# Kernel tuning notes

Measured on AMD Instinct MI355X. Metric: run time of the kernel, lower is better.

Reference implementation:

```python
import jax, jax.numpy as jnp
from jax import lax
import numpy as np

T, B, C, H = 2048, 512, 8, 20  # seq_len, batch, input channels, hidden size


def _lstm_layer(x_seq, W_ih, W_hh, b_ih, b_hh):
    """One unidirectional LSTM layer, PyTorch gate order (i, f, g, o).
    x_seq: [T, B, in], W_ih: [4H, in], W_hh: [4H, H]. Returns h sequence [T, B, H]."""
    Hh = W_hh.shape[1]
    # Precompute input contribution for all timesteps (batched GEMM, off the scan critical path)
    gx = jnp.einsum('tbc,gc->tbg', x_seq, W_ih) + b_ih + b_hh  # [T, B, 4H]

    def step(carry, g_t):
        h, c = carry
        g = g_t + h @ W_hh.T  # [B, 4H]
        i, f, gg, o = jnp.split(g, 4, axis=-1)
        i = jax.nn.sigmoid(i)
        f = jax.nn.sigmoid(f)
        gg = jnp.tanh(gg)
        o = jax.nn.sigmoid(o)
        c = f * c + i * gg
        h = o * jnp.tanh(c)
        return (h, c), h

    b = x_seq.shape[1]
    h0 = jnp.zeros((b, Hh), x_seq.dtype)
    c0 = jnp.zeros((b, Hh), x_seq.dtype)
    _, ys = lax.scan(step, (h0, c0), gx)
    return ys


def setup_inputs() -> dict:
    key = jax.random.key(0)
    ks = jax.random.split(key, 9)
    s = 1.0 / np.sqrt(H)  # PyTorch LSTM init scale
    return {
        'x': jax.random.normal(ks[0], (T, B, C), jnp.float32),
        'W_ih0': jax.random.uniform(ks[1], (4 * H, C), jnp.float32, -s, s),
        'W_hh0': jax.random.uniform(ks[2], (4 * H, H), jnp.float32, -s, s),
        'b_ih0': jax.random.uniform(ks[3], (4 * H,), jnp.float32, -s, s),
        'b_hh0': jax.random.uniform(ks[4], (4 * H,), jnp.float32, -s, s),
        'W_ih1': jax.random.uniform(ks[5], (4 * H, H), jnp.float32, -s, s),
        'W_hh1': jax.random.uniform(ks[6], (4 * H, H), jnp.float32, -s, s),
        'b_ih1': jax.random.uniform(ks[7], (4 * H,), jnp.float32, -s, s),
        'b_hh1': jax.random.uniform(ks[8], (4 * H,), jnp.float32, -s, s),
    }


def reference(x, W_ih0, W_hh0, b_ih0, b_hh0, W_ih1, W_hh1, b_ih1, b_hh1):
    # 2-layer LSTM with zero initial states; forward returns the full output sequence
    # (the fc head in the original module is unused in forward()).
    h1 = _lstm_layer(x, W_ih0, W_hh0, b_ih0, b_hh0)   # [T, B, H]
    out = _lstm_layer(h1, W_ih1, W_hh1, b_ih1, b_hh1)  # [T, B, H]
    return out
```

## Files before the change

kernel.cpp:

```cpp
#include <hip/hip_runtime.h>

namespace {

typedef float v2f __attribute__((ext_vector_type(2)));

constexpr int T_SEQ = 2048;
constexpr int B_SZ  = 512;
constexpr int C_IN  = 8;
constexpr int H_SZ  = 20;
constexpr int P_LEN = 16;
constexpr int N_PH  = T_SEQ / P_LEN;
constexpr int RING  = 2 * P_LEN;
constexpr float LOG2E = 1.44269504088896340736f;

__device__ __forceinline__ float rlane(float v, int lane) {
  return __int_as_float(__builtin_amdgcn_readlane(__float_as_int(v), lane));
}

template<int S>
__device__ __forceinline__ float quad_bcast(float v) {
  return __int_as_float(__builtin_amdgcn_update_dpp(
      __float_as_int(v), __float_as_int(v), S * 0x55, 0xF, 0xF, true));
}

__device__ __forceinline__ v2f fma2(v2f a, v2f b, v2f c) {
  return __builtin_elementwise_fma(a, b, c);
}
__device__ __forceinline__ v2f splat2(float s) { v2f r; r.x = s; r.y = s; return r; }
__device__ __forceinline__ v2f zero2() { v2f r; r.x = 0.f; r.y = 0.f; return r; }

__device__ __forceinline__ v2f act2(v2f a, float cm, float am, float ad) {
  float ex = __builtin_amdgcn_exp2f(a.x * cm);
  float ey = __builtin_amdgcn_exp2f(a.y * cm);
  float sx = __builtin_amdgcn_rcpf(1.0f + ex);
  float sy = __builtin_amdgcn_rcpf(1.0f + ey);
  v2f r; r.x = __fmaf_rn(sx, am, ad); r.y = __fmaf_rn(sy, am, ad);
  return r;
}

__device__ __forceinline__ float fast_tanh(float a) {
  float e = __builtin_amdgcn_exp2f(a * (-2.0f * LOG2E));
  float s = __builtin_amdgcn_rcpf(1.0f + e);
  return __fmaf_rn(s, 2.0f, -1.0f);
}

#define H_BCAST(ha, hb, k) (((k) < 16) ? rlane((ha), 4 * (k)) : rlane((hb), 4 * ((k) - 16)))

__global__ __attribute__((amdgpu_flat_work_group_size(128, 128),
                          amdgpu_waves_per_eu(1, 1)))
void lstm2_pk(const float* __restrict__ x,
              const float* __restrict__ Wih0, const float* __restrict__ Whh0,
              const float* __restrict__ bih0, const float* __restrict__ bhh0,
              const float* __restrict__ Wih1, const float* __restrict__ Whh1,
              const float* __restrict__ bih1, const float* __restrict__ bhh1,
              float* __restrict__ out)
{
  __shared__ __align__(16) float hbuf[RING][H_SZ];
  __shared__ __align__(16) float xbuf[2][P_LEN * C_IN];

  const int tid = threadIdx.x;
  const int wv  = tid >> 6;
  const int l   = tid & 63;
  const int b   = blockIdx.x;
  const int k1  = l >> 2;
  const int g   = l & 3;
  const int k2  = 16 + (k1 & 3);
  const int j1  = g * H_SZ + k1;
  const int j2  = g * H_SZ + k2;

  const bool  isg = (g == 2);
  const float cm  = isg ? (-2.0f * LOG2E) : (-LOG2E);
  const float am  = isg ?  2.0f : 1.0f;
  const float ad  = isg ? -1.0f : 0.0f;

  if (wv == 0) {
    v2f wx1[C_IN / 2], wx2[C_IN / 2];
    v2f wh[H_SZ];
#pragma unroll
    for (int t = 0; t < C_IN / 2; ++t) {
      wx1[t].x = Wih0[j1 * C_IN + 2 * t]; wx1[t].y = Wih0[j1 * C_IN + 2 * t + 1];
      wx2[t].x = Wih0[j2 * C_IN + 2 * t]; wx2[t].y = Wih0[j2 * C_IN + 2 * t + 1];
    }
#pragma unroll
    for (int k = 0; k < H_SZ; ++k) {
      wh[k].x = Whh0[j1 * H_SZ + k]; wh[k].y = Whh0[j2 * H_SZ + k];
    }
    v2f bias2; bias2.x = bih0[j1] + bhh0[j1]; bias2.y = bih0[j2] + bhh0[j2];

    float ha = 0.f, ca = 0.f, hb = 0.f, cb = 0.f;

    const float* xl = x + (size_t)(l >> 3) * (B_SZ * C_IN) + b * C_IN + (l & 7);
    const size_t halfph = (size_t)8 * B_SZ * C_IN;
    const size_t phstr  = (size_t)P_LEN * B_SZ * C_IN;

    {
      float v0 = xl[0], v1 = xl[halfph];
      xbuf[0][l] = v0; xbuf[0][64 + l] = v1;
    }
    float n0 = xl[phstr], n1 = xl[phstr + halfph];

    for (int p = 0; p <= N_PH; ++p) {
      if (p < N_PH) {
        const int buf = p & 1;
        float4 xc0 = ((const float4*)&xbuf[buf][0])[0];
        float4 xc1 = ((const float4*)&xbuf[buf][0])[1];
        for (int j = 0; j < P_LEN; ++j) {
          const int n = p * P_LEN + j;
          v2f xp[4];
          xp[0].x = xc0.x; xp[0].y = xc0.y; xp[1].x = xc0.z; xp[1].y = xc0.w;
          xp[2].x = xc1.x; xp[2].y = xc1.y; xp[3].x = xc1.z; xp[3].y = xc1.w;
          if (j + 1 < P_LEN) {
            xc0 = ((const float4*)&xbuf[buf][(j + 1) * C_IN])[0];
            xc1 = ((const float4*)&xbuf[buf][(j + 1) * C_IN])[1];
          }

          v2f A0 = bias2, A1 = zero2();
#pragma unroll
          for (int k = 0; k < H_SZ; k += 2) {
            float h0 = H_BCAST(ha, hb, k);
            float h1 = H_BCAST(ha, hb, k + 1);
            A0 = fma2(wh[k],     splat2(h0), A0);
            A1 = fma2(wh[k + 1], splat2(h1), A1);
          }
          v2f X1 = zero2(), X2 = zero2();
#pragma unroll
          for (int t = 0; t < C_IN / 2; ++t) {
            X1 = fma2(wx1[t], xp[t], X1);
            X2 = fma2(wx2[t], xp[t], X2);
          }
          v2f A = A0 + A1;
          A.x += X1.x + X1.y;
          A.y += X2.x + X2.y;

          v2f act = act2(A, cm, am, ad);
          float iv = quad_bcast<0>(act.x), fv = quad_bcast<1>(act.x);
          float gv = quad_bcast<2>(act.x), ov = quad_bcast<3>(act.x);
          ca = __fmaf_rn(fv, ca, iv * gv);
          ha = ov * fast_tanh(ca);
          iv = quad_bcast<0>(act.y); fv = quad_bcast<1>(act.y);
          gv = quad_bcast<2>(act.y); ov = quad_bcast<3>(act.y);
          cb = __fmaf_rn(fv, cb, iv * gv);
          hb = ov * fast_tanh(cb);

          const int slot = n & (RING - 1);
          if (g == 0) {
            hbuf[slot][k1] = ha;
            if (k1 < 4) hbuf[slot][16 + k1] = hb;
          }
        }
        if (p + 1 < N_PH) { xbuf[(p + 1) & 1][l] = n0; xbuf[(p + 1) & 1][64 + l] = n1; }
        if (p + 2 < N_PH) {
          n0 = xl[(size_t)(p + 2) * phstr];
          n1 = xl[(size_t)(p + 2) * phstr + halfph];
        }
      }
      __syncthreads();
    }
  } else {
    v2f wy1[H_SZ / 2], wy2[H_SZ / 2];
    v2f wq[H_SZ];
#pragma unroll
    for (int t = 0; t < H_SZ / 2; ++t) {
      wy1[t].x = Wih1[j1 * H_SZ + 2 * t]; wy1[t].y = Wih1[j1 * H_SZ + 2 * t + 1];
      wy2[t].x = Wih1[j2 * H_SZ + 2 * t]; wy2[t].y = Wih1[j2 * H_SZ + 2 * t + 1];
    }
#pragma unroll
    for (int k = 0; k < H_SZ; ++k) {
      wq[k].x = Whh1[j1 * H_SZ + k]; wq[k].y = Whh1[j2 * H_SZ + k];
    }
    v2f bias2; bias2.x = bih1[j1] + bhh1[j1]; bias2.y = bih1[j2] + bhh1[j2];

    float ha = 0.f, ca = 0.f, hb = 0.f, cb = 0.f;
    float* op = out + b * H_SZ;

    auto stepW1 = [&](int n, const float4 (&yq)[5]) {
      v2f yp[H_SZ / 2];
      yp[0].x = yq[0].x; yp[0].y = yq[0].y; yp[1].x = yq[0].z; yp[1].y = yq[0].w;
      yp[2].x = yq[1].x; yp[2].y = yq[1].y; yp[3].x = yq[1].z; yp[3].y = yq[1].w;
      yp[4].x = yq[2].x; yp[4].y = yq[2].y; yp[5].x = yq[2].z; yp[5].y = yq[2].w;
      yp[6].x = yq[3].x; yp[6].y = yq[3].y; yp[7].x = yq[3].z; yp[7].y = yq[3].w;
      yp[8].x = yq[4].x; yp[8].y = yq[4].y; yp[9].x = yq[4].z; yp[9].y = yq[4].w;

      v2f Y1a = zero2(), Y1b = zero2(), Y2a = zero2(), Y2b = zero2();
#pragma unroll
      for (int t = 0; t < H_SZ / 2; t += 2) {
        Y1a = fma2(wy1[t],     yp[t],     Y1a);
        Y2a = fma2(wy2[t],     yp[t],     Y2a);
        Y1b = fma2(wy1[t + 1], yp[t + 1], Y1b);
        Y2b = fma2(wy2[t + 1], yp[t + 1], Y2b);
      }
      v2f Q0 = bias2, Q1 = zero2();
#pragma unroll
      for (int k = 0; k < H_SZ; k += 2) {
        float q0 = H_BCAST(ha, hb, k);
        float q1 = H_BCAST(ha, hb, k + 1);
        Q0 = fma2(wq[k],     splat2(q0), Q0);
        Q1 = fma2(wq[k + 1], splat2(q1), Q1);
      }
      v2f A = Q0 + Q1;
      v2f Y1 = Y1a + Y1b, Y2 = Y2a + Y2b;
      A.x += Y1.x + Y1.y;
      A.y += Y2.x + Y2.y;

      v2f act = act2(A, cm, am, ad);
      float iv = quad_bcast<0>(act.x), fv = quad_bcast<1>(act.x);
      float gv = quad_bcast<2>(act.x), ov = quad_bcast<3>(act.x);
      ca = __fmaf_rn(fv, ca, iv * gv);
      ha = ov * fast_tanh(ca);
      iv = quad_bcast<0>(act.y); fv = quad_bcast<1>(act.y);
      gv = quad_bcast<2>(act.y); ov = quad_bcast<3>(act.y);
      cb = __fmaf_rn(fv, cb, iv * gv);
      hb = ov * fast_tanh(cb);

      if (g == 0) {
        op[k1] = ha;
        if (k1 < 4) op[16 + k1] = hb;
      }
      op += B_SZ * H_SZ;
    };

    for (int p = 0; p <= N_PH; ++p) {
      if (p >= 1) {
        const int base = (p - 1) * P_LEN;
        float4 yA[5], yB[5];
        {
          const float4* s = (const float4*)hbuf[base & (RING - 1)];
          yA[0] = s[0]; yA[1] = s[1]; yA[2] = s[2]; yA[3] = s[3]; yA[4] = s[4];
        }
        {
          const float4* s = (const float4*)hbuf[(base + 1) & (RING - 1)];
          yB[0] = s[0]; yB[1] = s[1]; yB[2] = s[2]; yB[3] = s[3]; yB[4] = s[4];
        }
        for (int jj = 0; jj < P_LEN; jj += 2) {
          stepW1(base + jj, yA);
          if (jj + 2 < P_LEN) {
            const float4* s = (const float4*)hbuf[(base + jj + 2) & (RING - 1)];
            yA[0] = s[0]; yA[1] = s[1]; yA[2] = s[2]; yA[3] = s[3]; yA[4] = s[4];
          }
          stepW1(base + jj + 1, yB);
          if (jj + 3 < P_LEN) {
            const float4* s = (const float4*)hbuf[(base + jj + 3) & (RING - 1)];
            yB[0] = s[0]; yB[1] = s[1]; yB[2] = s[2]; yB[3] = s[3]; yB[4] = s[4];
          }
        }
      }
      __syncthreads();
    }
  }
}

}

extern "C" void kernel_launch(void* const* d_in, const int* in_sizes, int n_in,
                              void* d_out, int out_size, void* d_ws, size_t ws_size,
                              hipStream_t stream) {
  const float* x    = (const float*)d_in[0];
  const float* Wih0 = (const float*)d_in[1];
  const float* Whh0 = (const float*)d_in[2];
  const float* bih0 = (const float*)d_in[3];
  const float* bhh0 = (const float*)d_in[4];
  const float* Wih1 = (const float*)d_in[5];
  const float* Whh1 = (const float*)d_in[6];
  const float* bih1 = (const float*)d_in[7];
  const float* bhh1 = (const float*)d_in[8];
  float* out = (float*)d_out;

  hipLaunchKernelGGL(lstm2_pk, dim3(B_SZ), dim3(128), 0, stream,
                     x, Wih0, Whh0, bih0, bhh0, Wih1, Whh1, bih1, bhh1, out);
}
```

Before: 706.8 us.

## Broadcast recurrent hidden state through LDS instead of readlane, lengthen phases

Replaces the per-step readlane broadcasts of the hidden state (20 scalar readlanes per step) with LDS writes and vectorized v2f LDS reads of the previous h. Layer 0 reads it from the ring buffer and layer 1 from a new double-buffered h1buf. Phase length doubles to 32 to halve block barriers. Within one wave the LDS round trip relies on in-order LDS behaviour, and it adds store-to-load latency to the serial recurrence.

New measurement: 761.5 us. +7.7%, slower.

```diff
diff --git a/kernel.cpp b/kernel.cpp
--- a/kernel.cpp
+++ b/kernel.cpp
@@ -8,14 +8,10 @@
 constexpr int B_SZ  = 512;
 constexpr int C_IN  = 8;
 constexpr int H_SZ  = 20;
-constexpr int P_LEN = 16;
+constexpr int P_LEN = 32;
 constexpr int N_PH  = T_SEQ / P_LEN;
 constexpr int RING  = 2 * P_LEN;
 constexpr float LOG2E = 1.44269504088896340736f;
-
-__device__ __forceinline__ float rlane(float v, int lane) {
-  return __int_as_float(__builtin_amdgcn_readlane(__float_as_int(v), lane));
-}
 
 template<int S>
 __device__ __forceinline__ float quad_bcast(float v) {
@@ -26,7 +22,6 @@
 __device__ __forceinline__ v2f fma2(v2f a, v2f b, v2f c) {
   return __builtin_elementwise_fma(a, b, c);
 }
-__device__ __forceinline__ v2f splat2(float s) { v2f r; r.x = s; r.y = s; return r; }
 __device__ __forceinline__ v2f zero2() { v2f r; r.x = 0.f; r.y = 0.f; return r; }
 
 __device__ __forceinline__ v2f act2(v2f a, float cm, float am, float ad) {
@@ -44,18 +39,17 @@
   return __fmaf_rn(s, 2.0f, -1.0f);
 }
 
-#define H_BCAST(ha, hb, k) (((k) < 16) ? rlane((ha), 4 * (k)) : rlane((hb), 4 * ((k) - 16)))
-
 __global__ __attribute__((amdgpu_flat_work_group_size(128, 128),
                           amdgpu_waves_per_eu(1, 1)))
-void lstm2_pk(const float* __restrict__ x,
-              const float* __restrict__ Wih0, const float* __restrict__ Whh0,
-              const float* __restrict__ bih0, const float* __restrict__ bhh0,
-              const float* __restrict__ Wih1, const float* __restrict__ Whh1,
-              const float* __restrict__ bih1, const float* __restrict__ bhh1,
-              float* __restrict__ out)
+void lstm2_lds(const float* __restrict__ x,
+               const float* __restrict__ Wih0, const float* __restrict__ Whh0,
+               const float* __restrict__ bih0, const float* __restrict__ bhh0,
+               const float* __restrict__ Wih1, const float* __restrict__ Whh1,
+               const float* __restrict__ bih1, const float* __restrict__ bhh1,
+               float* __restrict__ out)
 {
   __shared__ __align__(16) float hbuf[RING][H_SZ];
+  __shared__ __align__(16) float h1buf[2][H_SZ];
   __shared__ __align__(16) float xbuf[2][P_LEN * C_IN];
 
   const int tid = threadIdx.x;
@@ -75,72 +69,70 @@
 
   if (wv == 0) {
     v2f wx1[C_IN / 2], wx2[C_IN / 2];
-    v2f wh[H_SZ];
+    v2f wh1[H_SZ / 2], wh2[H_SZ / 2];
 #pragma unroll
     for (int t = 0; t < C_IN / 2; ++t) {
       wx1[t].x = Wih0[j1 * C_IN + 2 * t]; wx1[t].y = Wih0[j1 * C_IN + 2 * t + 1];
       wx2[t].x = Wih0[j2 * C_IN + 2 * t]; wx2[t].y = Wih0[j2 * C_IN + 2 * t + 1];
     }
 #pragma unroll
-    for (int k = 0; k < H_SZ; ++k) {
-      wh[k].x = Whh0[j1 * H_SZ + k]; wh[k].y = Whh0[j2 * H_SZ + k];
-    }
-    v2f bias2; bias2.x = bih0[j1] + bhh0[j1]; bias2.y = bih0[j2] + bhh0[j2];
-
-    float ha = 0.f, ca = 0.f, hb = 0.f, cb = 0.f;
-
-    const float* xl = x + (size_t)(l >> 3) * (B_SZ * C_IN) + b * C_IN + (l & 7);
-    const size_t halfph = (size_t)8 * B_SZ * C_IN;
-    const size_t phstr  = (size_t)P_LEN * B_SZ * C_IN;
-
+    for (int t = 0; t < H_SZ / 2; ++t) {
+      wh1[t].x = Whh0[j1 * H_SZ + 2 * t]; wh1[t].y = Whh0[j1 * H_SZ + 2 * t + 1];
+      wh2[t].x = Whh0[j2 * H_SZ + 2 * t]; wh2[t].y = Whh0[j2 * H_SZ + 2 * t + 1];
+    }
+    const float bs1 = bih0[j1] + bhh0[j1];
+    const float bs2 = bih0[j2] + bhh0[j2];
+
+    float ca = 0.f, cb = 0.f;
+
+    if (l < H_SZ) hbuf[RING - 1][l] = 0.f;
+
+    const float* xl = x + (size_t)(l >> 3) * (B_SZ * C_IN)
+                        + (size_t)b * C_IN + (l & 7);
+    const size_t ustr  = (size_t)8 * B_SZ * C_IN;
+    const size_t phstr = (size_t)P_LEN * B_SZ * C_IN;
     {
-      float v0 = xl[0], v1 = xl[halfph];
-      xbuf[0][l] = v0; xbuf[0][64 + l] = v1;
-    }
-    float n0 = xl[phstr], n1 = xl[phstr + halfph];
+      float a0 = xl[0], a1 = xl[ustr], a2 = xl[2 * ustr], a3 = xl[3 * ustr];
+      xbuf[0][l] = a0; xbuf[0][64 + l] = a1;
+      xbuf[0][128 + l] = a2; xbuf[0][192 + l] = a3;
+    }
+    float xr0 = xl[phstr], xr1 = xl[phstr + ustr],
+          xr2 = xl[phstr + 2 * ustr], xr3 = xl[phstr + 3 * ustr];
 
     for (int p = 0; p <= N_PH; ++p) {
       if (p < N_PH) {
         const int buf = p & 1;
-        float4 xc0 = ((const float4*)&xbuf[buf][0])[0];
-        float4 xc1 = ((const float4*)&xbuf[buf][0])[1];
         for (int j = 0; j < P_LEN; ++j) {
           const int n = p * P_LEN + j;
-          v2f xp[4];
-          xp[0].x = xc0.x; xp[0].y = xc0.y; xp[1].x = xc0.z; xp[1].y = xc0.w;
-          xp[2].x = xc1.x; xp[2].y = xc1.y; xp[3].x = xc1.z; xp[3].y = xc1.w;
-          if (j + 1 < P_LEN) {
-            xc0 = ((const float4*)&xbuf[buf][(j + 1) * C_IN])[0];
-            xc1 = ((const float4*)&xbuf[buf][(j + 1) * C_IN])[1];
-          }
-
-          v2f A0 = bias2, A1 = zero2();
-#pragma unroll
-          for (int k = 0; k < H_SZ; k += 2) {
-            float h0 = H_BCAST(ha, hb, k);
-            float h1 = H_BCAST(ha, hb, k + 1);
-            A0 = fma2(wh[k],     splat2(h0), A0);
-            A1 = fma2(wh[k + 1], splat2(h1), A1);
-          }
-          v2f X1 = zero2(), X2 = zero2();
-#pragma unroll
-          for (int t = 0; t < C_IN / 2; ++t) {
-            X1 = fma2(wx1[t], xp[t], X1);
-            X2 = fma2(wx2[t], xp[t], X2);
-          }
-          v2f A = A0 + A1;
-          A.x += X1.x + X1.y;
-          A.y += X2.x + X2.y;
-
-          v2f act = act2(A, cm, am, ad);
+          const v2f* xp = (const v2f*)&xbuf[buf][j * C_IN];
+          const v2f* hp = (const v2f*)hbuf[(n + RING - 1) & (RING - 1)];
+
+          v2f A0, A1, A2, A3;
+          A0.x = bs1; A0.y = 0.f; A1 = zero2();
+          A2.x = bs2; A2.y = 0.f; A3 = zero2();
+          A0 = fma2(wx1[0], xp[0], A0);  A2 = fma2(wx2[0], xp[0], A2);
+          A1 = fma2(wx1[1], xp[1], A1);  A3 = fma2(wx2[1], xp[1], A3);
+          A0 = fma2(wx1[2], xp[2], A0);  A2 = fma2(wx2[2], xp[2], A2);
+          A1 = fma2(wx1[3], xp[3], A1);  A3 = fma2(wx2[3], xp[3], A3);
+#pragma unroll
+          for (int t = 0; t < H_SZ / 2; t += 2) {
+            A0 = fma2(wh1[t],     hp[t],     A0);
+            A2 = fma2(wh2[t],     hp[t],     A2);
+            A1 = fma2(wh1[t + 1], hp[t + 1], A1);
+            A3 = fma2(wh2[t + 1], hp[t + 1], A3);
+          }
+          v2f S1 = A0 + A1, S2 = A2 + A3;
+          v2f G; G.x = S1.x + S1.y; G.y = S2.x + S2.y;
+
+          v2f act = act2(G, cm, am, ad);
           float iv = quad_bcast<0>(act.x), fv = quad_bcast<1>(act.x);
           float gv = quad_bcast<2>(act.x), ov = quad_bcast<3>(act.x);
           ca = __fmaf_rn(fv, ca, iv * gv);
-          ha = ov * fast_tanh(ca);
+          float ha = ov * fast_tanh(ca);
           iv = quad_bcast<0>(act.y); fv = quad_bcast<1>(act.y);
           gv = quad_bcast<2>(act.y); ov = quad_bcast<3>(act.y);
           cb = __fmaf_rn(fv, cb, iv * gv);
-          hb = ov * fast_tanh(cb);
+          float hb = ov * fast_tanh(cb);
 
           const int slot = n & (RING - 1);
           if (g == 0) {
@@ -148,100 +140,80 @@
             if (k1 < 4) hbuf[slot][16 + k1] = hb;
           }
         }
-        if (p + 1 < N_PH) { xbuf[(p + 1) & 1][l] = n0; xbuf[(p + 1) & 1][64 + l] = n1; }
+        if (p + 1 < N_PH) {
+          const int nb = (p + 1) & 1;
+          xbuf[nb][l] = xr0; xbuf[nb][64 + l] = xr1;
+          xbuf[nb][128 + l] = xr2; xbuf[nb][192 + l] = xr3;
+        }
         if (p + 2 < N_PH) {
-          n0 = xl[(size_t)(p + 2) * phstr];
-          n1 = xl[(size_t)(p + 2) * phstr + halfph];
+          const size_t o = (size_t)(p + 2) * phstr;
+          xr0 = xl[o]; xr1 = xl[o + ustr];
+          xr2 = xl[o + 2 * ustr]; xr3 = xl[o + 3 * ustr];
         }
       }
       __syncthreads();
     }
   } else {
     v2f wy1[H_SZ / 2], wy2[H_SZ / 2];
-    v2f wq[H_SZ];
+    v2f wq1[H_SZ / 2], wq2[H_SZ / 2];
 #pragma unroll
     for (int t = 0; t < H_SZ / 2; ++t) {
       wy1[t].x = Wih1[j1 * H_SZ + 2 * t]; wy1[t].y = Wih1[j1 * H_SZ + 2 * t + 1];
       wy2[t].x = Wih1[j2 * H_SZ + 2 * t]; wy2[t].y = Wih1[j2 * H_SZ + 2 * t + 1];
-    }
-#pragma unroll
-    for (int k = 0; k < H_SZ; ++k) {
-      wq[k].x = Whh1[j1 * H_SZ + k]; wq[k].y = Whh1[j2 * H_SZ + k];
-    }
-    v2f bias2; bias2.x = bih1[j1] + bhh1[j1]; bias2.y = bih1[j2] + bhh1[j2];
-
-    float ha = 0.f, ca = 0.f, hb = 0.f, cb = 0.f;
-    float* op = out + b * H_SZ;
-
-    auto stepW1 = [&](int n, const float4 (&yq)[5]) {
-      v2f yp[H_SZ / 2];
-      yp[0].x = yq[0].x; yp[0].y = yq[0].y; yp[1].x = yq[0].z; yp[1].y = yq[0].w;
-      yp[2].x = yq[1].x; yp[2].y = yq[1].y; yp[3].x = yq[1].z; yp[3].y = yq[1].w;
-      yp[4].x = yq[2].x; yp[4].y = yq[2].y; yp[5].x = yq[2].z; yp[5].y = yq[2].w;
-      yp[6].x = yq[3].x; yp[6].y = yq[3].y; yp[7].x = yq[3].z; yp[7].y = yq[3].w;
-      yp[8].x = yq[4].x; yp[8].y = yq[4].y; yp[9].x = yq[4].z; yp[9].y = yq[4].w;
-
-      v2f Y1a = zero2(), Y1b = zero2(), Y2a = zero2(), Y2b = zero2();
-#pragma unroll
-      for (int t = 0; t < H_SZ / 2; t += 2) {
-        Y1a = fma2(wy1[t],     yp[t],     Y1a);
-        Y2a = fma2(wy2[t],     yp[t],     Y2a);
-        Y1b = fma2(wy1[t + 1], yp[t + 1], Y1b);
-        Y2b = fma2(wy2[t + 1], yp[t + 1], Y2b);
-      }
-      v2f Q0 = bias2, Q1 = zero2();
-#pragma unroll
-      for (int k = 0; k < H_SZ; k += 2) {
-        float q0 = H_BCAST(ha, hb, k);
-        float q1 = H_BCAST(ha, hb, k + 1);
-        Q0 = fma2(wq[k],     splat2(q0), Q0);
-        Q1 = fma2(wq[k + 1], splat2(q1), Q1);
-      }
-      v2f A = Q0 + Q1;
-      v2f Y1 = Y1a + Y1b, Y2 = Y2a + Y2b;
-      A.x += Y1.x + Y1.y;
-      A.y += Y2.x + Y2.y;
-
-      v2f act = act2(A, cm, am, ad);
-      float iv = quad_bcast<0>(act.x), fv = quad_bcast<1>(act.x);
-      float gv = quad_bcast<2>(act.x), ov = quad_bcast<3>(act.x);
-      ca = __fmaf_rn(fv, ca, iv * gv);
-      ha = ov * fast_tanh(ca);
-      iv = quad_bcast<0>(act.y); fv = quad_bcast<1>(act.y);
-      gv = quad_bcast<2>(act.y); ov = quad_bcast<3>(act.y);
-      cb = __fmaf_rn(fv, cb, iv * gv);
-      hb = ov * fast_tanh(cb);
-
-      if (g == 0) {
-        op[k1] = ha;
-        if (k1 < 4) op[16 + k1] = hb;
-      }
-      op += B_SZ * H_SZ;
-    };
+      wq1[t].x = Whh1[j1 * H_SZ + 2 * t]; wq1[t].y = Whh1[j1 * H_SZ + 2 * t + 1];
+      wq2[t].x = Whh1[j2 * H_SZ + 2 * t]; wq2[t].y = Whh1[j2 * H_SZ + 2 * t + 1];
+    }
+    const float bs1 = bih1[j1] + bhh1[j1];
+    const float bs2 = bih1[j2] + bhh1[j2];
+
+    float ca = 0.f, cb = 0.f;
+    float* op = out + (size_t)b * H_SZ;
+
+    if (l < H_SZ) h1buf[1][l] = 0.f;
 
     for (int p = 0; p <= N_PH; ++p) {
       if (p >= 1) {
         const int base = (p - 1) * P_LEN;
-        float4 yA[5], yB[5];
-        {
-          const float4* s = (const float4*)hbuf[base & (RING - 1)];
-          yA[0] = s[0]; yA[1] = s[1]; yA[2] = s[2]; yA[3] = s[3]; yA[4] = s[4];
-        }
-        {
-          const float4* s = (const float4*)hbuf[(base + 1) & (RING - 1)];
-          yB[0] = s[0]; yB[1] = s[1]; yB[2] = s[2]; yB[3] = s[3]; yB[4] = s[4];
-        }
-        for (int jj = 0; jj < P_LEN; jj += 2) {
-          stepW1(base + jj, yA);
-          if (jj + 2 < P_LEN) {
-            const float4* s = (const float4*)hbuf[(base + jj + 2) & (RING - 1)];
-            yA[0] = s[0]; yA[1] = s[1]; yA[2] = s[2]; yA[3] = s[3]; yA[4] = s[4];
-          }
-          stepW1(base + jj + 1, yB);
-          if (jj + 3 < P_LEN) {
-            const float4* s = (const float4*)hbuf[(base + jj + 3) & (RING - 1)];
-            yB[0] = s[0]; yB[1] = s[1]; yB[2] = s[2]; yB[3] = s[3]; yB[4] = s[4];
-          }
+        for (int j = 0; j < P_LEN; ++j) {
+          const int m = base + j;
+          const v2f* yp = (const v2f*)hbuf[m & (RING - 1)];
+          const v2f* qp = (const v2f*)h1buf[(m + 1) & 1];
+
+          v2f A0, A1, A2, A3, A4, A5, A6, A7;
+          A0.x = bs1; A0.y = 0.f; A1 = zero2(); A2 = zero2(); A3 = zero2();
+          A4.x = bs2; A4.y = 0.f; A5 = zero2(); A6 = zero2(); A7 = zero2();
+#pragma unroll
+          for (int t = 0; t < H_SZ / 2; t += 2) {
+            A0 = fma2(wy1[t],     yp[t],     A0);
+            A4 = fma2(wy2[t],     yp[t],     A4);
+            A1 = fma2(wy1[t + 1], yp[t + 1], A1);
+            A5 = fma2(wy2[t + 1], yp[t + 1], A5);
+            A2 = fma2(wq1[t],     qp[t],     A2);
+            A6 = fma2(wq2[t],     qp[t],     A6);
+            A3 = fma2(wq1[t + 1], qp[t + 1], A3);
+            A7 = fma2(wq2[t + 1], qp[t + 1], A7);
+          }
+          v2f S1 = (A0 + A1) + (A2 + A3);
+          v2f S2 = (A4 + A5) + (A6 + A7);
+          v2f G; G.x = S1.x + S1.y; G.y = S2.x + S2.y;
+
+          v2f act = act2(G, cm, am, ad);
+          float iv = quad_bcast<0>(act.x), fv = quad_bcast<1>(act.x);
+          float gv = quad_bcast<2>(act.x), ov = quad_bcast<3>(act.x);
+          ca = __fmaf_rn(fv, ca, iv * gv);
+          float ha = ov * fast_tanh(ca);
+          iv = quad_bcast<0>(act.y); fv = quad_bcast<1>(act.y);
+          gv = quad_bcast<2>(act.y); ov = quad_bcast<3>(act.y);
+          cb = __fmaf_rn(fv, cb, iv * gv);
+          float hb = ov * fast_tanh(cb);
+
+          if (g == 0) {
+            h1buf[m & 1][k1] = ha;
+            if (k1 < 4) h1buf[m & 1][16 + k1] = hb;
+            op[k1] = ha;
+            if (k1 < 4) op[16 + k1] = hb;
+          }
+          op += (size_t)B_SZ * H_SZ;
         }
       }
       __syncthreads();
@@ -265,6 +237,6 @@
   const float* bhh1 = (const float*)d_in[8];
   float* out = (float*)d_out;
 
-  hipLaunchKernelGGL(lstm2_pk, dim3(B_SZ), dim3(128), 0, stream,
+  hipLaunchKernelGGL(lstm2_lds, dim3(B_SZ), dim3(128), 0, stream,
                      x, Wih0, Whh0, bih0, bhh0, Wih1, Whh1, bih1, bhh1, out);
 }
```
